# Performance work log

Hardware: AMD Instinct MI355X
Metric: run time of the kernel (lower is better)

Reference implementation:

```python
import jax, jax.numpy as jnp
import numpy as np

B, CIN, COUT, W0, MX, MY, NL, H, WW = 8, 2, 1, 64, 16, 16, 4, 256, 256


def setup_inputs() -> dict:
    key = jax.random.key(0)
    ks = jax.random.split(key, 8)
    scale = 1.0 / (W0 * W0)  # torch: 1/(in_channels*out_channels)
    return {
        "x": jax.random.normal(ks[0], (B, CIN, H, WW), jnp.float32),
        "in_w": 0.1 * jax.random.normal(ks[1], (W0, CIN), jnp.float32),
        "in_b": jnp.zeros((W0,), jnp.float32),
        "spec_wr": scale * jax.random.normal(ks[2], (NL, W0, W0, MX, MY), jnp.float32),
        "spec_wi": scale * jax.random.normal(ks[3], (NL, W0, W0, MX, MY), jnp.float32),
        "pw_w": 0.05 * jax.random.normal(ks[4], (NL, W0, W0), jnp.float32),
        "pw_b": jnp.zeros((NL, W0), jnp.float32),
        "o1_w": 0.1 * jax.random.normal(ks[5], (W0 // 2, W0), jnp.float32),
        "o1_b": jnp.zeros((W0 // 2,), jnp.float32),
        "o2_w": 0.1 * jax.random.normal(ks[6], (COUT, W0 // 2), jnp.float32),
        "o2_b": jnp.zeros((COUT,), jnp.float32),
    }


def _conv1x1(x, w, b):
    # x: [B,C,H,W], w: [O,C], b: [O]  (1x1 Conv2d == channel matmul)
    return jnp.einsum('oc,bchw->bohw', w, x) + b[None, :, None, None]


def _spectral_conv(x, wr, wi):
    # x: [B,C_in,H,W]; wr/wi: [C_in,C_out,MX,MY]
    Bq, C, Hh, Ww = x.shape
    x_ft = jnp.fft.rfft2(x, norm='ortho')              # [B,C,H,W//2+1] complex64
    mx = min(wr.shape[2], Hh)
    my = min(wr.shape[3], Ww // 2 + 1)
    w = (wr[:, :, :mx, :my] + 1j * wi[:, :, :mx, :my]).astype(jnp.complex64)
    # complex mode-limited GEMM: sum over input channels
    out = jnp.einsum('bixy,ioxy->boxy', x_ft[:, :, :mx, :my], w)
    out_ft = jnp.zeros((Bq, wr.shape[1], Hh, Ww // 2 + 1), jnp.complex64)
    out_ft = out_ft.at[:, :, :mx, :my].set(out)
    return jnp.fft.irfft2(out_ft, s=(Hh, Ww), norm='ortho')


def reference(x, in_w, in_b, spec_wr, spec_wi, pw_w, pw_b, o1_w, o1_b, o2_w, o2_b):
    gelu = lambda t: jax.nn.gelu(t, approximate=False)  # torch nn.GELU default = exact erf
    h = _conv1x1(x, in_w, in_b)
    for l in range(NL):
        x1 = _spectral_conv(h, spec_wr[l], spec_wi[l])
        x2 = _conv1x1(h, pw_w[l], pw_b[l])
        h = gelu(x1 + x2)
    h = gelu(_conv1x1(h, o1_w, o1_b))
    return _conv1x1(h, o2_w, o2_b)
```

## Files before the change

### kernel.cpp

```cpp
#include <hip/hip_runtime.h>
#include <math.h>


#define NLAYER 4

#define OFF_H     0L
#define OFF_A2    16777216L
#define OFF_XFP   18874368L
#define OFF_YA    33554432L
#define OFF_XF    37748736L
#define OFF_TAB   38010880L
#define OFF_O1W   38011136L
#define OFF_TRIG  38013184L
#define OFF_WT    38017280L
#define OFF_TRIGT 38025472L
#define WS_FLOATS 38029568L

typedef __attribute__((ext_vector_type(8))) short short8;
typedef __attribute__((ext_vector_type(4))) float f32x4;

__device__ __forceinline__ unsigned short f2bf(float f) {
  unsigned int u = __float_as_uint(f);
  u += 0x7FFF + ((u >> 16) & 1);
  return (unsigned short)(u >> 16);
}

__global__ void k_init(float* __restrict__ ws, const float* __restrict__ pw_w,
                       const float* __restrict__ o1_w) {
  float* costab = ws + OFF_TAB;
  unsigned short* o1wbf = (unsigned short*)(ws + OFF_O1W);
  unsigned short* trig = (unsigned short*)(ws + OFF_TRIG);
  unsigned short* wt = (unsigned short*)(ws + OFF_WT);
  unsigned short* trigT = (unsigned short*)(ws + OFF_TRIGT);
  int t = blockIdx.x * blockDim.x + threadIdx.x;
  int stride = gridDim.x * blockDim.x;
  for (int m = t; m < 256; m += stride)
    costab[m] = (float)cos((double)m * (3.14159265358979323846 / 128.0));
  for (int idx = t; idx < 32 * 64; idx += stride)
    o1wbf[idx] = f2bf(o1_w[idx]);
  for (int idx = t; idx < 256 * 32; idx += stride) {
    int y = idx >> 5, k = idx & 31;
    int mm = ((k & 15) * y) & 255;
    double ang = (double)mm * (3.14159265358979323846 / 128.0);
    double v = (k < 16) ? cos(ang) : sin(ang);
    trig[idx] = f2bf((float)v);
  }
  for (int idx = t; idx < 32 * 256; idx += stride) {
    int r = idx >> 8, y = idx & 255;
    int mm = ((r & 15) * y) & 255;
    double ang = (double)mm * (3.14159265358979323846 / 128.0);
    double v = (r < 16) ? cos(ang) : sin(ang);
    trigT[idx] = f2bf((float)v);
  }
  for (int idx = t; idx < NLAYER * 64 * 64; idx += stride)
    wt[idx] = f2bf(pw_w[idx]);
}

__global__ void __launch_bounds__(256) k_in(const float* __restrict__ x,
                                            const float* __restrict__ in_w,
                                            const float* __restrict__ in_b,
                                            unsigned short* __restrict__ hb) {
  long tid = (long)blockIdx.x * 256 + threadIdx.x;
  int o0 = (int)(tid & 15) << 2;
  long p = tid >> 4;
  long b = p >> 16; long xy = p & 65535;
  float x0 = x[b * 131072 + xy];
  float x1 = x[b * 131072 + 65536 + xy];
  ushort4 r;
  r.x = f2bf(in_b[o0]     + in_w[o0 * 2]     * x0 + in_w[o0 * 2 + 1] * x1);
  r.y = f2bf(in_b[o0 + 1] + in_w[o0 * 2 + 2] * x0 + in_w[o0 * 2 + 3] * x1);
  r.z = f2bf(in_b[o0 + 2] + in_w[o0 * 2 + 4] * x0 + in_w[o0 * 2 + 5] * x1);
  r.w = f2bf(in_b[o0 + 3] + in_w[o0 * 2 + 6] * x0 + in_w[o0 * 2 + 7] * x1);
  *(ushort4*)(hb + (p << 6) + o0) = r;
}

__global__ void __launch_bounds__(256) k_f1(const unsigned short* __restrict__ hb,
                                            const unsigned short* __restrict__ trigT,
                                            float* __restrict__ Y) {
  __shared__ unsigned short St[64 * 256];
  int t = threadIdx.x;
  long row = blockIdx.x;
  const unsigned short* hrow = hb + (row << 14);
  #pragma unroll
  for (int kk = 0; kk < 8; ++kk) {
    int idx8 = t + (kk << 8);
    short8 v = *(const short8*)(hrow + (idx8 << 3));
    int y = idx8 >> 3, c0 = (idx8 & 7) << 3;
    int yb = y >> 3, y7 = y & 7;
    #pragma unroll
    for (int e = 0; e < 8; ++e) {
      int c = c0 + e;
      St[(c << 8) + (((yb ^ (c >> 3)) & 31) << 3) + y7] = (unsigned short)v[e];
    }
  }
  __syncthreads();
  int lane = t & 63;
  int wid = t >> 6;
  int kq = lane >> 4, n = lane & 15;
  #pragma unroll
  for (int pp = 0; pp < 2; ++pp) {
    int p = wid + (pp << 2);
    int mt = p & 1, nt = p >> 1;
    int trow = (mt << 4) + n;
    int c = (nt << 4) + n;
    const unsigned short* abase = trigT + (trow << 8) + (kq << 3);
    f32x4 acc = {0.0f, 0.0f, 0.0f, 0.0f};
    #pragma unroll
    for (int k0 = 0; k0 < 8; ++k0) {
      short8 af = *(const short8*)(abase + (k0 << 5));
      int yb = (k0 << 2) + kq;
      short8 bf = *(const short8*)(&St[(c << 8) + (((yb ^ (c >> 3)) & 31) << 3)]);
      acc = __builtin_amdgcn_mfma_f32_16x16x32_bf16(af, bf, acc, 0, 0, 0);
    }
    float sgn = mt ? -0.0625f : 0.0625f;
    float* yp = Y + (row << 11) + (kq << 9) + (c << 1) + mt;
    #pragma unroll
    for (int r = 0; r < 4; ++r)
      yp[r << 7] = acc[r] * sgn;
  }
}

__global__ void __launch_bounds__(256) k_f2(const float* __restrict__ Y,
                                            const float* __restrict__ costab,
                                            float* __restrict__ Xfp) {
  __shared__ float T[256];
  int t = threadIdx.x;
  T[t] = costab[t];
  __syncthreads();
  int s = blockIdx.x >> 9;
  int blk = blockIdx.x & 511;
  int bk = blk >> 2;
  int b = bk >> 4, ky = bk & 15;
  int c = ((blk & 3) << 4) + (t & 15);
  int kx = t >> 4;
  int x0 = s << 6;
  const float* ybase = Y + ((long)b * 4096 + ky) * 128 + c * 2 + (long)x0 * 2048;
  float ar = 0.0f, ai = 0.0f;
  int m = (kx * x0) & 255;
  #pragma unroll 4
  for (int x = 0; x < 64; ++x) {
    float2 v = *(const float2*)(ybase + (long)x * 2048);
    float cv = T[m], sv = T[(m + 192) & 255];
    ar += v.x * cv + v.y * sv;
    ai += v.y * cv - v.x * sv;
    m = (m + kx) & 255;
  }
  float* o = Xfp + (long)s * 262144 + ((long)b * 64 + c) * 512 + (kx * 16 + ky) * 2;
  o[0] = ar * 0.0625f;
  o[1] = ai * 0.0625f;
}

__global__ void __launch_bounds__(256) k_xsum(const float* __restrict__ Xfp,
                                              float* __restrict__ Xf) {
  long i = ((long)blockIdx.x * 256 + threadIdx.x) << 2;
  f32x4 a = *(const f32x4*)(Xfp + i);
  f32x4 b = *(const f32x4*)(Xfp + 262144 + i);
  f32x4 c = *(const f32x4*)(Xfp + 524288 + i);
  f32x4 d = *(const f32x4*)(Xfp + 786432 + i);
  f32x4 ab = a + b;
  f32x4 cd = c + d;
  *(f32x4*)(Xf + i) = ab + cd;
}

__global__ void __launch_bounds__(512) k_spec(const float* __restrict__ Xf,
                                              const float* __restrict__ wr,
                                              const float* __restrict__ wi,
                                              const float* __restrict__ costab,
                                              unsigned short* __restrict__ A2) {
  __shared__ float T[256];
  __shared__ float Gr[256], Gi[256];
  __shared__ float Pr[512], Pi[512];
  int t = threadIdx.x;
  if (t < 256) T[t] = costab[t];
  int b = blockIdx.x >> 6, o = blockIdx.x & 63;
  {
    int m = t & 255, h = t >> 8;
    float gr = 0, gi = 0;
    const float* xb = Xf + (long)b * 32768 + m * 2 + (long)(h << 5) * 512;
    const float* wrb = wr + (long)o * 256 + m + (long)(h << 5) * 16384;
    const float* wib = wi + (long)o * 256 + m + (long)(h << 5) * 16384;
    for (int i = 0; i < 32; ++i) {
      float xr = xb[(long)i * 512], xi = xb[(long)i * 512 + 1];
      float wrv = wrb[(long)i * 16384], wiv = wib[(long)i * 16384];
      gr += xr * wrv - xi * wiv;
      gi += xr * wiv + xi * wrv;
    }
    Pr[t] = gr; Pi[t] = gi;
  }
  __syncthreads();
  if (t < 256) {
    Gr[t] = Pr[t] + Pr[t + 256];
    Gi[t] = Pi[t] + Pi[t + 256];
  }
  __syncthreads();
  int x = t & 255, kyh = t >> 8;
  float ar[8], ai[8];
  #pragma unroll
  for (int r = 0; r < 8; ++r) { ar[r] = 0.0f; ai[r] = 0.0f; }
  for (int kx = 0; kx < 16; ++kx) {
    int mm = (kx * x) & 255;
    float cv = T[mm], sv = T[(mm + 192) & 255];
    int gb = (kx << 4) + (kyh << 3);
    #pragma unroll
    for (int r = 0; r < 8; ++r) {
      float gr = Gr[gb + r], gi = Gi[gb + r];
      ar[r] += gr * cv - gi * sv;
      ai[r] += gr * sv + gi * cv;
    }
  }
  unsigned short* ab = A2 + ((long)(b * 256 + x) << 11) + (o << 5) + (kyh << 3);
  short8 va, vb;
  #pragma unroll
  for (int r = 0; r < 8; ++r) {
    float sc = (kyh == 0 && r == 0) ? 0.00390625f : 0.0078125f;
    va[r] = (short)f2bf(ar[r] * sc);
    vb[r] = (short)f2bf(-ai[r] * sc);
  }
  *(short8*)ab = va;
  *(short8*)(ab + 16) = vb;
}

__global__ void __launch_bounds__(512) k_pw(unsigned short* __restrict__ hb,
                                            const unsigned short* __restrict__ A2,
                                            const unsigned short* __restrict__ Wt,
                                            const unsigned short* __restrict__ trig,
                                            const unsigned short* __restrict__ trigT,
                                            const float* __restrict__ pw_b,
                                            float* __restrict__ Y,
                                            int do_f1) {
  __shared__ unsigned short S[256 * 64];
  int t = threadIdx.x;
  long row = blockIdx.x;
  int lane = t & 63;
  int wid = t >> 6;
  int kq = lane >> 4, n = lane & 15;
  int half = wid >> 2;
  int o = ((wid & 3) << 4) + n;
  const unsigned short* wrow = Wt + (o << 6) + (kq << 3);
  short8 B0 = *(const short8*)(wrow);
  short8 B1 = *(const short8*)(wrow + 32);
  short8 B2 = *(const short8*)(A2 + (row << 11) + (o << 5) + (kq << 3));
  float bias = pw_b[o];
  const unsigned short* hrow = hb + (row << 14);
  #pragma unroll
  for (int k = 0; k < 4; ++k) {
    int idx8 = t + (k << 9);
    short8 v = *(const short8*)(hrow + (idx8 << 3));
    int yy = idx8 >> 3, c8 = idx8 & 7;
    *(short8*)(&S[(yy << 6) + (((c8 ^ yy) & 7) << 3)]) = v;
  }
  __syncthreads();
  int s0 = (kq ^ n) & 7;
  ushort4 res[8];
  #pragma unroll
  for (int i = 0; i < 8; ++i) {
    int m0 = i << 4;
    int yrow = (half << 7) + m0 + n;
    const unsigned short* srow = &S[yrow << 6];
    short8 a0 = *(const short8*)(srow + (s0 << 3));
    short8 a1 = *(const short8*)(srow + ((s0 ^ 4) << 3));
    short8 a2 = *(const short8*)(trig + (yrow << 5) + (kq << 3));
    f32x4 acc = {0.0f, 0.0f, 0.0f, 0.0f};
    acc = __builtin_amdgcn_mfma_f32_16x16x32_bf16(a0, B0, acc, 0, 0, 0);
    acc = __builtin_amdgcn_mfma_f32_16x16x32_bf16(a1, B1, acc, 0, 0, 0);
    acc = __builtin_amdgcn_mfma_f32_16x16x32_bf16(a2, B2, acc, 0, 0, 0);
    float v0 = acc[0] + bias;
    v0 = 0.5f * v0 * (1.0f + erff(v0 * 0.70710678118654752f));
    float v1 = acc[1] + bias;
    v1 = 0.5f * v1 * (1.0f + erff(v1 * 0.70710678118654752f));
    float v2 = acc[2] + bias;
    v2 = 0.5f * v2 * (1.0f + erff(v2 * 0.70710678118654752f));
    float v3 = acc[3] + bias;
    v3 = 0.5f * v3 * (1.0f + erff(v3 * 0.70710678118654752f));
    res[i].x = f2bf(v0); res[i].y = f2bf(v1);
    res[i].z = f2bf(v2); res[i].w = f2bf(v3);
    int y0 = (half << 7) + m0 + (kq << 2);
    unsigned short* ob = hb + (row << 14) + ((long)y0 << 6) + o;
    ob[0] = res[i].x; ob[64] = res[i].y; ob[128] = res[i].z; ob[192] = res[i].w;
  }
  if (do_f1) {
    __syncthreads();
    #pragma unroll
    for (int i = 0; i < 8; ++i) {
      int y0 = (half << 7) + (i << 4) + (kq << 2);
      int yb = y0 >> 3;
      *(ushort4*)(&S[(o << 8) + (((yb ^ (o >> 3)) & 31) << 3) + (y0 & 7)]) = res[i];
    }
    __syncthreads();
    int mt = wid & 1, nt = wid >> 1;
    int trow = (mt << 4) + n;
    int c = (nt << 4) + n;
    const unsigned short* abase = trigT + (trow << 8) + (kq << 3);
    f32x4 acc = {0.0f, 0.0f, 0.0f, 0.0f};
    #pragma unroll
    for (int k0 = 0; k0 < 8; ++k0) {
      short8 af = *(const short8*)(abase + (k0 << 5));
      int yb = (k0 << 2) + kq;
      short8 bf = *(const short8*)(&S[(c << 8) + (((yb ^ (c >> 3)) & 31) << 3)]);
      acc = __builtin_amdgcn_mfma_f32_16x16x32_bf16(af, bf, acc, 0, 0, 0);
    }
    float sgn = mt ? -0.0625f : 0.0625f;
    float* yp = Y + (row << 11) + (kq << 9) + (c << 1) + mt;
    #pragma unroll
    for (int r = 0; r < 4; ++r)
      yp[r << 7] = acc[r] * sgn;
  }
}

__global__ void __launch_bounds__(256) k_out(const unsigned short* __restrict__ hb,
                                             const unsigned short* __restrict__ o1wbf,
                                             const float* __restrict__ o1_b,
                                             const float* __restrict__ o2_w,
                                             const float* __restrict__ o2_b,
                                             float* __restrict__ out) {
  __shared__ unsigned short S[128 * 88];
  int t = threadIdx.x;
  long row = blockIdx.x >> 1;
  int half = blockIdx.x & 1;
  const unsigned short* hbase = hb + (row << 14) + (half << 13);
  #pragma unroll
  for (int k = 0; k < 4; ++k) {
    int idx8 = t + (k << 8);
    short8 v = *(const short8*)(hbase + (idx8 << 3));
    int yy = idx8 >> 3, c8 = idx8 & 7;
    *(short8*)(&S[yy * 88 + (c8 << 3)]) = v;
  }
  int lane = t & 63;
  int kq = lane >> 4;
  int n = lane & 15;
  int wid = t >> 6;
  const unsigned short* w0 = o1wbf + (n << 6) + (kq << 3);
  const unsigned short* w1 = o1wbf + ((n + 16) << 6) + (kq << 3);
  short8 B0a = *(const short8*)(w0);
  short8 B0b = *(const short8*)(w0 + 32);
  short8 B1a = *(const short8*)(w1);
  short8 B1b = *(const short8*)(w1 + 32);
  float b0 = o1_b[n], b1 = o1_b[n + 16];
  float g0 = o2_w[n], g1 = o2_w[n + 16];
  float ob2 = o2_b[0];
  __syncthreads();
  float* outp = out + row * 256 + (half << 7);
  #pragma unroll
  for (int mt = 0; mt < 2; ++mt) {
    int m0 = (wid << 5) + (mt << 4);
    const unsigned short* srow = &S[(m0 + n) * 88 + (kq << 3)];
    short8 a0 = *(const short8*)(srow);
    short8 a1 = *(const short8*)(srow + 32);
    f32x4 c0 = {0.0f, 0.0f, 0.0f, 0.0f}, c1 = {0.0f, 0.0f, 0.0f, 0.0f};
    c0 = __builtin_amdgcn_mfma_f32_16x16x32_bf16(a0, B0a, c0, 0, 0, 0);
    c0 = __builtin_amdgcn_mfma_f32_16x16x32_bf16(a1, B0b, c0, 0, 0, 0);
    c1 = __builtin_amdgcn_mfma_f32_16x16x32_bf16(a0, B1a, c1, 0, 0, 0);
    c1 = __builtin_amdgcn_mfma_f32_16x16x32_bf16(a1, B1b, c1, 0, 0, 0);
    #pragma unroll
    for (int r = 0; r < 4; ++r) {
      float v0 = c0[r] + b0;
      v0 = 0.5f * v0 * (1.0f + erff(v0 * 0.70710678118654752f));
      float v1 = c1[r] + b1;
      v1 = 0.5f * v1 * (1.0f + erff(v1 * 0.70710678118654752f));
      float s = v0 * g0 + v1 * g1;
      s += __shfl_xor(s, 1);
      s += __shfl_xor(s, 2);
      s += __shfl_xor(s, 4);
      s += __shfl_xor(s, 8);
      if (n == 0) outp[m0 + (kq << 2) + r] = s + ob2;
    }
  }
}

extern "C" void kernel_launch(void* const* d_in, const int* in_sizes, int n_in,
                              void* d_out, int out_size, void* d_ws, size_t ws_size,
                              hipStream_t stream) {
  const float* x       = (const float*)d_in[0];
  const float* in_w    = (const float*)d_in[1];
  const float* in_b    = (const float*)d_in[2];
  const float* spec_wr = (const float*)d_in[3];
  const float* spec_wi = (const float*)d_in[4];
  const float* pw_w    = (const float*)d_in[5];
  const float* pw_b    = (const float*)d_in[6];
  const float* o1_w    = (const float*)d_in[7];
  const float* o1_b    = (const float*)d_in[8];
  const float* o2_w    = (const float*)d_in[9];
  const float* o2_b    = (const float*)d_in[10];
  float* ws = (float*)d_ws;
  unsigned short* hb = (unsigned short*)(ws + OFF_H);
  unsigned short* A2 = (unsigned short*)(ws + OFF_A2);
  float* Xfp    = ws + OFF_XFP;
  float* Y      = ws + OFF_YA;
  float* Xf     = ws + OFF_XF;
  float* costab = ws + OFF_TAB;
  unsigned short* o1wbf = (unsigned short*)(ws + OFF_O1W);
  unsigned short* trig = (unsigned short*)(ws + OFF_TRIG);
  unsigned short* wt   = (unsigned short*)(ws + OFF_WT);
  unsigned short* trigT = (unsigned short*)(ws + OFF_TRIGT);
  float* out = (float*)d_out;

  k_init<<<73, 256, 0, stream>>>(ws, pw_w, o1_w);
  k_in<<<32768, 256, 0, stream>>>(x, in_w, in_b, hb);
  k_f1<<<2048, 256, 0, stream>>>(hb, trigT, Y);
  for (int l = 0; l < NLAYER; ++l) {
    k_f2<<<2048, 256, 0, stream>>>(Y, costab, Xfp);
    k_xsum<<<256, 256, 0, stream>>>(Xfp, Xf);
    k_spec<<<512, 512, 0, stream>>>(Xf, spec_wr + (long)l * 1048576,
                                    spec_wi + (long)l * 1048576, costab, A2);
    k_pw<<<2048, 512, 0, stream>>>(hb, A2, wt + l * 4096, trig, trigT,
                                   pw_b + l * 64, Y, (l < NLAYER - 1) ? 1 : 0);
  }
  k_out<<<4096, 256, 0, stream>>>(hb, o1wbf, o1_b, o2_w, o2_b, out);
}
```

Before: 469.0 us.

## Fuse input projection into first DFT, fold partial-sum reduction into spectral kernel, pair rows in pointwise

The input 1x1 conv is now computed inside k_f1 from the raw input, so k_in is gone and its bf16 activation tensor is no longer round-tripped through memory. The separate k_xsum reduction is removed: k_spec reads the four partial spectra directly and sums them while loading. k_pw now processes two rows per block, prefetching both rows' activations into registers up front, which halves the grid and amortizes the weight loads. Together these remove several launches and a lot of global traffic. The cost is more register pressure in k_pw and a 4x read amplification of Xfp in k_spec, since every output-channel block re-reads and re-sums the partials.

```diff
diff --git a/kernel.cpp b/kernel.cpp
--- a/kernel.cpp
+++ b/kernel.cpp
@@ -8,7 +8,6 @@
 #define OFF_A2    16777216L
 #define OFF_XFP   18874368L
 #define OFF_YA    33554432L
-#define OFF_XF    37748736L
 #define OFF_TAB   38010880L
 #define OFF_O1W   38011136L
 #define OFF_TRIG  38013184L
@@ -56,42 +55,45 @@
     wt[idx] = f2bf(pw_w[idx]);
 }
 
-__global__ void __launch_bounds__(256) k_in(const float* __restrict__ x,
+__global__ void __launch_bounds__(256) k_f1(const float* __restrict__ x,
                                             const float* __restrict__ in_w,
                                             const float* __restrict__ in_b,
-                                            unsigned short* __restrict__ hb) {
-  long tid = (long)blockIdx.x * 256 + threadIdx.x;
-  int o0 = (int)(tid & 15) << 2;
-  long p = tid >> 4;
-  long b = p >> 16; long xy = p & 65535;
-  float x0 = x[b * 131072 + xy];
-  float x1 = x[b * 131072 + 65536 + xy];
-  ushort4 r;
-  r.x = f2bf(in_b[o0]     + in_w[o0 * 2]     * x0 + in_w[o0 * 2 + 1] * x1);
-  r.y = f2bf(in_b[o0 + 1] + in_w[o0 * 2 + 2] * x0 + in_w[o0 * 2 + 3] * x1);
-  r.z = f2bf(in_b[o0 + 2] + in_w[o0 * 2 + 4] * x0 + in_w[o0 * 2 + 5] * x1);
-  r.w = f2bf(in_b[o0 + 3] + in_w[o0 * 2 + 6] * x0 + in_w[o0 * 2 + 7] * x1);
-  *(ushort4*)(hb + (p << 6) + o0) = r;
-}
-
-__global__ void __launch_bounds__(256) k_f1(const unsigned short* __restrict__ hb,
                                             const unsigned short* __restrict__ trigT,
+                                            unsigned short* __restrict__ hb,
                                             float* __restrict__ Y) {
   __shared__ unsigned short St[64 * 256];
+  __shared__ float X0[256], X1[256];
   int t = threadIdx.x;
   long row = blockIdx.x;
-  const unsigned short* hrow = hb + (row << 14);
+  long b = row >> 8, xr = row & 255;
+  const float* xb = x + b * 131072 + (xr << 8);
+  X0[t] = xb[t];
+  X1[t] = xb[65536 + t];
+  int c0 = (t & 7) << 3;
+  float wv[16], bv[8];
+  #pragma unroll
+  for (int e = 0; e < 8; ++e) {
+    wv[2 * e]     = in_w[(c0 + e) * 2];
+    wv[2 * e + 1] = in_w[(c0 + e) * 2 + 1];
+    bv[e]         = in_b[c0 + e];
+  }
+  __syncthreads();
+  unsigned short* hrow = hb + (row << 14);
   #pragma unroll
   for (int kk = 0; kk < 8; ++kk) {
     int idx8 = t + (kk << 8);
-    short8 v = *(const short8*)(hrow + (idx8 << 3));
-    int y = idx8 >> 3, c0 = (idx8 & 7) << 3;
+    int y = idx8 >> 3;
+    float x0 = X0[y], x1 = X1[y];
     int yb = y >> 3, y7 = y & 7;
+    short8 v;
     #pragma unroll
     for (int e = 0; e < 8; ++e) {
       int c = c0 + e;
-      St[(c << 8) + (((yb ^ (c >> 3)) & 31) << 3) + y7] = (unsigned short)v[e];
+      unsigned short hv = f2bf(bv[e] + wv[2 * e] * x0 + wv[2 * e + 1] * x1);
+      v[e] = (short)hv;
+      St[(c << 8) + (((yb ^ (c >> 3)) & 31) << 3) + y7] = hv;
     }
+    *(short8*)(hrow + (idx8 << 3)) = v;
   }
   __syncthreads();
   int lane = t & 63;
@@ -150,19 +152,7 @@
   o[1] = ai * 0.0625f;
 }
 
-__global__ void __launch_bounds__(256) k_xsum(const float* __restrict__ Xfp,
-                                              float* __restrict__ Xf) {
-  long i = ((long)blockIdx.x * 256 + threadIdx.x) << 2;
-  f32x4 a = *(const f32x4*)(Xfp + i);
-  f32x4 b = *(const f32x4*)(Xfp + 262144 + i);
-  f32x4 c = *(const f32x4*)(Xfp + 524288 + i);
-  f32x4 d = *(const f32x4*)(Xfp + 786432 + i);
-  f32x4 ab = a + b;
-  f32x4 cd = c + d;
-  *(f32x4*)(Xf + i) = ab + cd;
-}
-
-__global__ void __launch_bounds__(512) k_spec(const float* __restrict__ Xf,
+__global__ void __launch_bounds__(512) k_spec(const float* __restrict__ Xfp,
                                               const float* __restrict__ wr,
                                               const float* __restrict__ wi,
                                               const float* __restrict__ costab,
@@ -176,11 +166,16 @@
   {
     int m = t & 255, h = t >> 8;
     float gr = 0, gi = 0;
-    const float* xb = Xf + (long)b * 32768 + m * 2 + (long)(h << 5) * 512;
+    const float* xb = Xfp + (long)b * 32768 + m * 2 + (long)(h << 5) * 512;
     const float* wrb = wr + (long)o * 256 + m + (long)(h << 5) * 16384;
     const float* wib = wi + (long)o * 256 + m + (long)(h << 5) * 16384;
     for (int i = 0; i < 32; ++i) {
-      float xr = xb[(long)i * 512], xi = xb[(long)i * 512 + 1];
+      float2 p0 = *(const float2*)(xb + (long)i * 512);
+      float2 p1 = *(const float2*)(xb + 262144 + (long)i * 512);
+      float2 p2 = *(const float2*)(xb + 524288 + (long)i * 512);
+      float2 p3 = *(const float2*)(xb + 786432 + (long)i * 512);
+      float xr = (p0.x + p1.x) + (p2.x + p3.x);
+      float xi = (p0.y + p1.y) + (p2.y + p3.y);
       float wrv = wrb[(long)i * 16384], wiv = wib[(long)i * 16384];
       gr += xr * wrv - xi * wiv;
       gi += xr * wiv + xi * wrv;
@@ -220,6 +215,68 @@
   *(short8*)(ab + 16) = vb;
 }
 
+#define PW_PROCESS(ROW, B2V)                                                   \
+  {                                                                            \
+    int s0 = (kq ^ n) & 7;                                                     \
+    ushort4 res[8];                                                            \
+    _Pragma("unroll")                                                          \
+    for (int i = 0; i < 8; ++i) {                                              \
+      int m0 = i << 4;                                                         \
+      int yrow = (half << 7) + m0 + n;                                         \
+      const unsigned short* srow = &S[yrow << 6];                              \
+      short8 a0 = *(const short8*)(srow + (s0 << 3));                          \
+      short8 a1 = *(const short8*)(srow + ((s0 ^ 4) << 3));                    \
+      short8 a2 = *(const short8*)(trig + (yrow << 5) + (kq << 3));            \
+      f32x4 acc = {0.0f, 0.0f, 0.0f, 0.0f};                                    \
+      acc = __builtin_amdgcn_mfma_f32_16x16x32_bf16(a0, B0, acc, 0, 0, 0);     \
+      acc = __builtin_amdgcn_mfma_f32_16x16x32_bf16(a1, B1, acc, 0, 0, 0);     \
+      acc = __builtin_amdgcn_mfma_f32_16x16x32_bf16(a2, B2V, acc, 0, 0, 0);    \
+      float v0 = acc[0] + bias;                                                \
+      v0 = 0.5f * v0 * (1.0f + erff(v0 * 0.70710678118654752f));               \
+      float v1 = acc[1] + bias;                                                \
+      v1 = 0.5f * v1 * (1.0f + erff(v1 * 0.70710678118654752f));               \
+      float v2 = acc[2] + bias;                                                \
+      v2 = 0.5f * v2 * (1.0f + erff(v2 * 0.70710678118654752f));               \
+      float v3 = acc[3] + bias;                                                \
+      v3 = 0.5f * v3 * (1.0f + erff(v3 * 0.70710678118654752f));               \
+      res[i].x = f2bf(v0); res[i].y = f2bf(v1);                                \
+      res[i].z = f2bf(v2); res[i].w = f2bf(v3);                                \
+      int y0 = (half << 7) + m0 + (kq << 2);                                   \
+      unsigned short* ob = hb + ((ROW) << 14) + ((long)y0 << 6) + o;           \
+      ob[0] = res[i].x; ob[64] = res[i].y;                                     \
+      ob[128] = res[i].z; ob[192] = res[i].w;                                  \
+    }                                                                          \
+    if (do_f1) {                                                               \
+      __syncthreads();                                                         \
+      _Pragma("unroll")                                                        \
+      for (int i = 0; i < 8; ++i) {                                            \
+        int y0 = (half << 7) + (i << 4) + (kq << 2);                           \
+        int yb = y0 >> 3;                                                      \
+        *(ushort4*)(&S[(o << 8) + (((yb ^ (o >> 3)) & 31) << 3) + (y0 & 7)]) = \
+            res[i];                                                            \
+      }                                                                        \
+      __syncthreads();                                                         \
+      int mt = wid & 1, nt = wid >> 1;                                         \
+      int trow = (mt << 4) + n;                                                \
+      int c = (nt << 4) + n;                                                   \
+      const unsigned short* abase = trigT + (trow << 8) + (kq << 3);           \
+      f32x4 acc = {0.0f, 0.0f, 0.0f, 0.0f};                                    \
+      _Pragma("unroll")                                                        \
+      for (int k0 = 0; k0 < 8; ++k0) {                                         \
+        short8 af = *(const short8*)(abase + (k0 << 5));                       \
+        int yb = (k0 << 2) + kq;                                               \
+        short8 bf =                                                            \
+            *(const short8*)(&S[(c << 8) + (((yb ^ (c >> 3)) & 31) << 3)]);    \
+        acc = __builtin_amdgcn_mfma_f32_16x16x32_bf16(af, bf, acc, 0, 0, 0);   \
+      }                                                                        \
+      float sgn = mt ? -0.0625f : 0.0625f;                                     \
+      float* yp = Y + ((ROW) << 11) + (kq << 9) + (c << 1) + mt;               \
+      _Pragma("unroll")                                                        \
+      for (int r = 0; r < 4; ++r)                                              \
+        yp[r << 7] = acc[r] * sgn;                                             \
+    }                                                                          \
+  }
+
 __global__ void __launch_bounds__(512) k_pw(unsigned short* __restrict__ hb,
                                             const unsigned short* __restrict__ A2,
                                             const unsigned short* __restrict__ Wt,
@@ -230,7 +287,7 @@
                                             int do_f1) {
   __shared__ unsigned short S[256 * 64];
   int t = threadIdx.x;
-  long row = blockIdx.x;
+  long row0 = (long)blockIdx.x << 1;
   int lane = t & 63;
   int wid = t >> 6;
   int kq = lane >> 4, n = lane & 15;
@@ -239,72 +296,34 @@
   const unsigned short* wrow = Wt + (o << 6) + (kq << 3);
   short8 B0 = *(const short8*)(wrow);
   short8 B1 = *(const short8*)(wrow + 32);
-  short8 B2 = *(const short8*)(A2 + (row << 11) + (o << 5) + (kq << 3));
+  short8 B2r0 = *(const short8*)(A2 + (row0 << 11) + (o << 5) + (kq << 3));
+  short8 B2r1 = *(const short8*)(A2 + ((row0 + 1) << 11) + (o << 5) + (kq << 3));
   float bias = pw_b[o];
-  const unsigned short* hrow = hb + (row << 14);
+  const unsigned short* hr = hb + (row0 << 14);
+  short8 v0[4], v1[4];
   #pragma unroll
   for (int k = 0; k < 4; ++k) {
     int idx8 = t + (k << 9);
-    short8 v = *(const short8*)(hrow + (idx8 << 3));
+    v0[k] = *(const short8*)(hr + (idx8 << 3));
+    v1[k] = *(const short8*)(hr + 16384 + (idx8 << 3));
+  }
+  #pragma unroll
+  for (int k = 0; k < 4; ++k) {
+    int idx8 = t + (k << 9);
     int yy = idx8 >> 3, c8 = idx8 & 7;
-    *(short8*)(&S[(yy << 6) + (((c8 ^ yy) & 7) << 3)]) = v;
-  }
-  __syncthreads();
-  int s0 = (kq ^ n) & 7;
-  ushort4 res[8];
-  #pragma unroll
-  for (int i = 0; i < 8; ++i) {
-    int m0 = i << 4;
-    int yrow = (half << 7) + m0 + n;
-    const unsigned short* srow = &S[yrow << 6];
-    short8 a0 = *(const short8*)(srow + (s0 << 3));
-    short8 a1 = *(const short8*)(srow + ((s0 ^ 4) << 3));
-    short8 a2 = *(const short8*)(trig + (yrow << 5) + (kq << 3));
-    f32x4 acc = {0.0f, 0.0f, 0.0f, 0.0f};
-    acc = __builtin_amdgcn_mfma_f32_16x16x32_bf16(a0, B0, acc, 0, 0, 0);
-    acc = __builtin_amdgcn_mfma_f32_16x16x32_bf16(a1, B1, acc, 0, 0, 0);
-    acc = __builtin_amdgcn_mfma_f32_16x16x32_bf16(a2, B2, acc, 0, 0, 0);
-    float v0 = acc[0] + bias;
-    v0 = 0.5f * v0 * (1.0f + erff(v0 * 0.70710678118654752f));
-    float v1 = acc[1] + bias;
-    v1 = 0.5f * v1 * (1.0f + erff(v1 * 0.70710678118654752f));
-    float v2 = acc[2] + bias;
-    v2 = 0.5f * v2 * (1.0f + erff(v2 * 0.70710678118654752f));
-    float v3 = acc[3] + bias;
-    v3 = 0.5f * v3 * (1.0f + erff(v3 * 0.70710678118654752f));
-    res[i].x = f2bf(v0); res[i].y = f2bf(v1);
-    res[i].z = f2bf(v2); res[i].w = f2bf(v3);
-    int y0 = (half << 7) + m0 + (kq << 2);
-    unsigned short* ob = hb + (row << 14) + ((long)y0 << 6) + o;
-    ob[0] = res[i].x; ob[64] = res[i].y; ob[128] = res[i].z; ob[192] = res[i].w;
-  }
-  if (do_f1) {
-    __syncthreads();
-    #pragma unroll
-    for (int i = 0; i < 8; ++i) {
-      int y0 = (half << 7) + (i << 4) + (kq << 2);
-      int yb = y0 >> 3;
-      *(ushort4*)(&S[(o << 8) + (((yb ^ (o >> 3)) & 31) << 3) + (y0 & 7)]) = res[i];
-    }
-    __syncthreads();
-    int mt = wid & 1, nt = wid >> 1;
-    int trow = (mt << 4) + n;
-    int c = (nt << 4) + n;
-    const unsigned short* abase = trigT + (trow << 8) + (kq << 3);
-    f32x4 acc = {0.0f, 0.0f, 0.0f, 0.0f};
-    #pragma unroll
-    for (int k0 = 0; k0 < 8; ++k0) {
-      short8 af = *(const short8*)(abase + (k0 << 5));
-      int yb = (k0 << 2) + kq;
-      short8 bf = *(const short8*)(&S[(c << 8) + (((yb ^ (c >> 3)) & 31) << 3)]);
-      acc = __builtin_amdgcn_mfma_f32_16x16x32_bf16(af, bf, acc, 0, 0, 0);
-    }
-    float sgn = mt ? -0.0625f : 0.0625f;
-    float* yp = Y + (row << 11) + (kq << 9) + (c << 1) + mt;
-    #pragma unroll
-    for (int r = 0; r < 4; ++r)
-      yp[r << 7] = acc[r] * sgn;
-  }
+    *(short8*)(&S[(yy << 6) + (((c8 ^ yy) & 7) << 3)]) = v0[k];
+  }
+  __syncthreads();
+  PW_PROCESS(row0, B2r0)
+  __syncthreads();
+  #pragma unroll
+  for (int k = 0; k < 4; ++k) {
+    int idx8 = t + (k << 9);
+    int yy = idx8 >> 3, c8 = idx8 & 7;
+    *(short8*)(&S[(yy << 6) + (((c8 ^ yy) & 7) << 3)]) = v1[k];
+  }
+  __syncthreads();
+  PW_PROCESS(row0 + 1, B2r1)
 }
 
 __global__ void __launch_bounds__(256) k_out(const unsigned short* __restrict__ hb,
@@ -386,7 +405,6 @@
   unsigned short* A2 = (unsigned short*)(ws + OFF_A2);
   float* Xfp    = ws + OFF_XFP;
   float* Y      = ws + OFF_YA;
-  float* Xf     = ws + OFF_XF;
   float* costab = ws + OFF_TAB;
   unsigned short* o1wbf = (unsigned short*)(ws + OFF_O1W);
   unsigned short* trig = (unsigned short*)(ws + OFF_TRIG);
@@ -395,14 +413,12 @@
   float* out = (float*)d_out;
 
   k_init<<<73, 256, 0, stream>>>(ws, pw_w, o1_w);
-  k_in<<<32768, 256, 0, stream>>>(x, in_w, in_b, hb);
-  k_f1<<<2048, 256, 0, stream>>>(hb, trigT, Y);
+  k_f1<<<2048, 256, 0, stream>>>(x, in_w, in_b, trigT, hb, Y);
   for (int l = 0; l < NLAYER; ++l) {
     k_f2<<<2048, 256, 0, stream>>>(Y, costab, Xfp);
-    k_xsum<<<256, 256, 0, stream>>>(Xfp, Xf);
-    k_spec<<<512, 512, 0, stream>>>(Xf, spec_wr + (long)l * 1048576,
+    k_spec<<<512, 512, 0, stream>>>(Xfp, spec_wr + (long)l * 1048576,
                                     spec_wi + (long)l * 1048576, costab, A2);
-    k_pw<<<2048, 512, 0, stream>>>(hb, A2, wt + l * 4096, trig, trigT,
+    k_pw<<<1024, 512, 0, stream>>>(hb, A2, wt + l * 4096, trig, trigT,
                                    pw_b + l * 64, Y, (l < NLAYER - 1) ? 1 : 0);
   }
   k_out<<<4096, 256, 0, stream>>>(hb, o1wbf, o1_b, o2_w, o2_b, out);
```

New measurement: 546.8 us. 16.6% more time.
